# Kernel tuning notes

Hardware: AMD Instinct MI355X
Metric: run time of the kernel (lower is better)

Reference implementation:

```python
import jax, jax.numpy as jnp
import numpy as np

B, HIDDEN, NH, MAX_S = 8, 4096, 32, 4096
HD = HIDDEN // NH  # 128
POS = 2047  # current cache write position (tokens 0..POS-1 already cached)


def setup_inputs() -> dict:
    key = jax.random.key(0)
    ks = jax.random.split(key, 7)
    x = jax.random.normal(ks[0], (B, 1, HIDDEN), dtype=jnp.float32)
    cached_k = jax.random.normal(ks[1], (B, NH, MAX_S, HD), dtype=jnp.float32)
    cached_v = jax.random.normal(ks[2], (B, NH, MAX_S, HD), dtype=jnp.float32)
    scale = 0.02
    wq = jax.random.normal(ks[3], (HIDDEN, HIDDEN), dtype=jnp.float32) * scale
    wk = jax.random.normal(ks[4], (HIDDEN, HIDDEN), dtype=jnp.float32) * scale
    wv = jax.random.normal(ks[5], (HIDDEN, HIDDEN), dtype=jnp.float32) * scale
    wo = jax.random.normal(ks[6], (HIDDEN, HIDDEN), dtype=jnp.float32) * scale
    return {"x": x, "cached_k": cached_k, "cached_v": cached_v,
            "wq": wq, "wk": wk, "wv": wv, "wo": wo, "cached_pos": POS}


def reference(x, cached_k, cached_v, wq, wk, wv, wo, cached_pos):
    # Decode step: seq_len == 1 (is_training=False path of the torch module).
    b, s, hidden = x.shape  # s == 1
    # Projections (torch Linear: y = x @ W.T), reshape to [B, H, 1, D]
    q = (x @ wq.T).reshape(b, s, NH, HD).transpose(0, 2, 1, 3)
    k = (x @ wk.T).reshape(b, s, NH, HD).transpose(0, 2, 1, 3)
    v = (x @ wv.T).reshape(b, s, NH, HD).transpose(0, 2, 1, 3)
    # Append new token's K/V into the cache at cached_pos (static python int)
    ck = cached_k.at[:, :, cached_pos, :].set(k[:, :, 0, :])
    cv = cached_v.at[:, :, cached_pos, :].set(v[:, :, 0, :])
    # Attend over the valid prefix [0, cached_pos]
    kk = ck[:, :, :cached_pos + 1, :]  # [B, H, T, D]
    vv = cv[:, :, :cached_pos + 1, :]
    scores = jnp.einsum('bhqd,bhkd->bhqk', q, kk) / jnp.sqrt(jnp.float32(HD))
    att = jax.nn.softmax(scores, axis=-1)  # stable softmax == module's _softmax
    out = jnp.einsum('bhqk,bhkd->bhqd', att, vv)  # [B, H, 1, D]
    out = out.transpose(0, 2, 1, 3).reshape(b, s, hidden)
    return out @ wo.T
```

## Files before the change

### kernel.cpp

```cpp
#include <hip/hip_runtime.h>
#include <cmath>

#define B_     8
#define NH_    32
#define HD_    128
#define HID_   4096
#define MAXS_  4096
#define NPAIR_ (B_ * NH_)
#define NSPLIT_ 4
#define PSTR_  132
#define NEG_BIG_ (-1e30f)

typedef float f4_ __attribute__((ext_vector_type(4)));

__device__ __forceinline__ f4_ ntload4(const float* p) {
  return __builtin_nontemporal_load((const f4_*)p);
}
__device__ __forceinline__ f4_ ld4(const float* p) {
  return *(const f4_*)p;
}
__device__ __forceinline__ float dot4(f4_ a, f4_ b) {
  f4_ m = a * b;
  return m.x + m.y + m.z + m.w;
}

__global__ __launch_bounds__(64) void gemv8(
    const float* __restrict__ W0, const float* __restrict__ W1,
    const float* __restrict__ W2, const float* __restrict__ x,
    float* __restrict__ out, int nb_per_mat)
{
  const int bid = blockIdx.x;
  const int m   = bid / nb_per_mat;
  const int r0  = (bid % nb_per_mat) * 8;
  const float* __restrict__ W = (m == 0) ? W0 : ((m == 1) ? W1 : W2);
  float* o = out + m * (B_ * HID_);

  const int lane = threadIdx.x;

  float acc[8][8];
#pragma unroll
  for (int r = 0; r < 8; ++r)
#pragma unroll
    for (int b = 0; b < 8; ++b) acc[r][b] = 0.f;

  const float* Wp = W + (size_t)r0 * HID_ + lane * 4;
  const float* xp = x + lane * 4;

  f4_ wa[8], wb[8];
#pragma unroll
  for (int r = 0; r < 8; ++r) wa[r] = ld4(Wp + (size_t)r * HID_);

#pragma unroll 1
  for (int u = 0; u < 16; u += 2) {
    {
      const int j = u * 256;
      f4_ xv[8];
#pragma unroll
      for (int b = 0; b < 8; ++b) xv[b] = ld4(xp + b * HID_ + j);
#pragma unroll
      for (int r = 0; r < 8; ++r)
        wb[r] = ld4(Wp + (size_t)r * HID_ + j + 256);
#pragma unroll
      for (int r = 0; r < 8; ++r)
#pragma unroll
        for (int b = 0; b < 8; ++b) acc[r][b] += dot4(wa[r], xv[b]);
    }
    {
      const int j = (u + 1) * 256;
      f4_ xv[8];
#pragma unroll
      for (int b = 0; b < 8; ++b) xv[b] = ld4(xp + b * HID_ + j);
      if (u + 2 < 16) {
#pragma unroll
        for (int r = 0; r < 8; ++r)
          wa[r] = ld4(Wp + (size_t)r * HID_ + j + 256);
      }
#pragma unroll
      for (int r = 0; r < 8; ++r)
#pragma unroll
        for (int b = 0; b < 8; ++b) acc[r][b] += dot4(wb[r], xv[b]);
    }
  }

#pragma unroll
  for (int r = 0; r < 8; ++r)
#pragma unroll
    for (int b = 0; b < 8; ++b) {
      float v = acc[r][b];
#pragma unroll
      for (int off = 32; off; off >>= 1) v += __shfl_xor(v, off);
      acc[r][b] = v;
    }

  if (lane == 0) {
#pragma unroll
    for (int r = 0; r < 8; ++r)
#pragma unroll
      for (int b = 0; b < 8; ++b)
        o[(size_t)b * HID_ + r0 + r] = acc[r][b];
  }
}

__global__ __launch_bounds__(256, 4) void attn_partial(
    const float* __restrict__ qkv, const float* __restrict__ ck,
    const float* __restrict__ cv, const int* __restrict__ ppos,
    float* __restrict__ part)
{
  __shared__ float sm[4], sl[4];
  __shared__ float sacc[4][HD_];

  const int pos  = *ppos;
  const int bid  = blockIdx.x;
  const int pair = bid >> 2;
  const int s    = bid & (NSPLIT_ - 1);
  const int b    = pair >> 5;
  const int h    = pair & (NH_ - 1);
  const int w    = threadIdx.x >> 6;
  const int lane = threadIdx.x & 63;
  const int half = lane >> 5, l32 = lane & 31;
  const int k0   = s * 512 + w * 128;

  float m = NEG_BIG_, l = 0.f;
  f4_ acc = (f4_)0.f;

  if (k0 <= pos) {
    const float scale = 0.08838834764831845f;
    f4_ q4 = ld4(qkv + b * HID_ + h * HD_ + l32 * 4) * scale;
    const float* kfresh = qkv + B_ * HID_     + b * HID_ + h * HD_;
    const float* vfresh = qkv + 2 * B_ * HID_ + b * HID_ + h * HD_;
    const float* ckh = ck + ((size_t)(b * NH_ + h)) * MAXS_ * HD_;
    const float* cvh = cv + ((size_t)(b * NH_ + h)) * MAXS_ * HD_;

    for (int c = 0; c < 8; ++c) {
      const int kbase = k0 + c * 16;
      f4_ k4[8], v4[8];
#pragma unroll
      for (int j = 0; j < 8; ++j) {
        const int ki = kbase + 2 * j + half;
        const float* kp = (ki == pos) ? kfresh : (ckh + (size_t)ki * HD_);
        const float* vp = (ki == pos) ? vfresh : (cvh + (size_t)ki * HD_);
        k4[j] = ntload4(kp + l32 * 4);
        v4[j] = ntload4(vp + l32 * 4);
      }

      float sc[8];
#pragma unroll
      for (int j = 0; j < 8; ++j) sc[j] = dot4(q4, k4[j]);

#pragma unroll
      for (int off = 16; off >= 1; off >>= 1)
#pragma unroll
        for (int j = 0; j < 8; ++j) sc[j] += __shfl_xor(sc[j], off);

#pragma unroll
      for (int j = 0; j < 8; ++j) {
        const int ki = kbase + 2 * j + half;
        if (ki > pos) sc[j] = -INFINITY;
      }

      const float cm = fmaxf(fmaxf(fmaxf(sc[0], sc[1]), fmaxf(sc[2], sc[3])),
                             fmaxf(fmaxf(sc[4], sc[5]), fmaxf(sc[6], sc[7])));
      const float mn   = fmaxf(m, cm);
      const float corr = __expf(m - mn);
      float p[8], ps = 0.f;
#pragma unroll
      for (int j = 0; j < 8; ++j) { p[j] = __expf(sc[j] - mn); ps += p[j]; }
      l = l * corr + ps;
      acc *= corr;
#pragma unroll
      for (int j = 0; j < 8; ++j) acc += p[j] * v4[j];
      m = mn;
    }
  }

  const float mo = __shfl_xor(m, 32);
  const float lo = __shfl_xor(l, 32);
  f4_ ao;
  ao.x = __shfl_xor(acc.x, 32); ao.y = __shfl_xor(acc.y, 32);
  ao.z = __shfl_xor(acc.z, 32); ao.w = __shfl_xor(acc.w, 32);
  const float mm = fmaxf(m, mo);
  const float w0 = __expf(m - mm), w1 = __expf(mo - mm);
  const float lm = l * w0 + lo * w1;
  f4_ am = acc * w0 + ao * w1;

  if (half == 0) {
    *(f4_*)&sacc[w][l32 * 4] = am;
    if (l32 == 0) { sm[w] = mm; sl[w] = lm; }
  }
  __syncthreads();

  if (threadIdx.x < 32) {
    const int t = threadIdx.x;
    float mg = NEG_BIG_;
#pragma unroll
    for (int u = 0; u < 4; ++u)
      if (sl[u] > 0.f) mg = fmaxf(mg, sm[u]);
    float ls = 0.f;
    f4_ o = (f4_)0.f;
#pragma unroll
    for (int u = 0; u < 4; ++u)
      if (sl[u] > 0.f) {
        const float wu = __expf(sm[u] - mg);
        ls += sl[u] * wu;
        o  += wu * ld4(&sacc[u][t * 4]);
      }
    float* pb = part + (size_t)bid * PSTR_;
    *(f4_*)(pb + 4 + t * 4) = o;
    if (t == 0) { pb[0] = (ls > 0.f) ? mg : NEG_BIG_; pb[1] = ls; }
  }
}

__global__ __launch_bounds__(128) void attn_combine(
    const float* __restrict__ part, float* __restrict__ attnout)
{
  const int pair = blockIdx.x;
  const int d    = threadIdx.x;
  const float* pb = part + (size_t)pair * NSPLIT_ * PSTR_;

  float mg = NEG_BIG_;
#pragma unroll
  for (int u = 0; u < NSPLIT_; ++u) {
    const float lu = pb[u * PSTR_ + 1];
    if (lu > 0.f) mg = fmaxf(mg, pb[u * PSTR_]);
  }
  float ls = 0.f, o = 0.f;
#pragma unroll
  for (int u = 0; u < NSPLIT_; ++u) {
    const float lu = pb[u * PSTR_ + 1];
    if (lu > 0.f) {
      const float wu = __expf(pb[u * PSTR_] - mg);
      ls += lu * wu;
      o  += wu * pb[u * PSTR_ + 4 + d];
    }
  }
  attnout[pair * HD_ + d] = o / ls;
}

extern "C" void kernel_launch(void* const* d_in, const int* in_sizes, int n_in,
                              void* d_out, int out_size, void* d_ws, size_t ws_size,
                              hipStream_t stream) {
  const float* x  = (const float*)d_in[0];
  const float* ck = (const float*)d_in[1];
  const float* cv = (const float*)d_in[2];
  const float* wq = (const float*)d_in[3];
  const float* wk = (const float*)d_in[4];
  const float* wv = (const float*)d_in[5];
  const float* wo = (const float*)d_in[6];
  const int* pos  = (const int*)d_in[7];
  float* out = (float*)d_out;
  float* ws  = (float*)d_ws;

  float* qkv     = ws;
  float* part    = ws + 3 * B_ * HID_;
  float* attnout = part + NPAIR_ * NSPLIT_ * PSTR_;

  gemv8<<<3 * 512, 64, 0, stream>>>(wq, wk, wv, x, qkv, 512);
  attn_partial<<<NPAIR_ * NSPLIT_, 256, 0, stream>>>(qkv, ck, cv, pos, part);
  attn_combine<<<NPAIR_, 128, 0, stream>>>(part, attnout);
  gemv8<<<512, 64, 0, stream>>>(wo, wo, wo, attnout, out, 512);
}
```

Baseline: 178.5 us.

## Split-K the QKV and output GEMVs to raise block count

The QKV projection now splits the reduction dimension in two and the output projection in four, so more workgroups each stream a shorter slice of the weight rows. The QKV partial sums are added inside the attention kernel when loading q and the fresh k/v, and the output partials are reduced by a new small sum kernel. The fresh-token substitution in attention changes from pointer selection to loading from the cache and then overwriting the value. The split costs extra partial-result traffic and one more kernel launch.

```diff
diff --git a/kernel.cpp b/kernel.cpp
--- a/kernel.cpp
+++ b/kernel.cpp
@@ -9,6 +9,7 @@
 #define NPAIR_ (B_ * NH_)
 #define NSPLIT_ 4
 #define PSTR_  132
+#define QS_    (3 * B_ * HID_)
 #define NEG_BIG_ (-1e30f)
 
 typedef float f4_ __attribute__((ext_vector_type(4)));
@@ -24,18 +25,22 @@
   return m.x + m.y + m.z + m.w;
 }
 
-__global__ __launch_bounds__(64) void gemv8(
+template<int NSL>
+__global__ __launch_bounds__(64) void gemv_ks(
     const float* __restrict__ W0, const float* __restrict__ W1,
     const float* __restrict__ W2, const float* __restrict__ x,
-    float* __restrict__ out, int nb_per_mat)
-{
-  const int bid = blockIdx.x;
-  const int m   = bid / nb_per_mat;
-  const int r0  = (bid % nb_per_mat) * 8;
+    float* __restrict__ out, int nb_per_mat, int n_inner, int part_stride)
+{
+  const int bid   = blockIdx.x;
+  const int ks    = bid / n_inner;
+  const int inner = bid % n_inner;
+  const int m     = inner / nb_per_mat;
+  const int r0    = (inner % nb_per_mat) * 8;
   const float* __restrict__ W = (m == 0) ? W0 : ((m == 1) ? W1 : W2);
-  float* o = out + m * (B_ * HID_);
+  float* o = out + (size_t)ks * part_stride + m * (B_ * HID_);
 
   const int lane = threadIdx.x;
+  const int kofs = ks * NSL * 256;
 
   float acc[8][8];
 #pragma unroll
@@ -43,15 +48,15 @@
 #pragma unroll
     for (int b = 0; b < 8; ++b) acc[r][b] = 0.f;
 
-  const float* Wp = W + (size_t)r0 * HID_ + lane * 4;
-  const float* xp = x + lane * 4;
+  const float* Wp = W + (size_t)r0 * HID_ + kofs + lane * 4;
+  const float* xp = x + kofs + lane * 4;
 
   f4_ wa[8], wb[8];
 #pragma unroll
   for (int r = 0; r < 8; ++r) wa[r] = ld4(Wp + (size_t)r * HID_);
 
 #pragma unroll 1
-  for (int u = 0; u < 16; u += 2) {
+  for (int u = 0; u < NSL; u += 2) {
     {
       const int j = u * 256;
       f4_ xv[8];
@@ -70,7 +75,7 @@
       f4_ xv[8];
 #pragma unroll
       for (int b = 0; b < 8; ++b) xv[b] = ld4(xp + b * HID_ + j);
-      if (u + 2 < 16) {
+      if (u + 2 < NSL) {
 #pragma unroll
         for (int r = 0; r < 8; ++r)
           wa[r] = ld4(Wp + (size_t)r * HID_ + j + 256);
@@ -99,6 +104,16 @@
       for (int b = 0; b < 8; ++b)
         o[(size_t)b * HID_ + r0 + r] = acc[r][b];
   }
+}
+
+__global__ __launch_bounds__(256) void sum4(
+    const float* __restrict__ part, float* __restrict__ out)
+{
+  const int gid = blockIdx.x * 256 + threadIdx.x;
+  const int i = gid * 4;
+  f4_ v = ld4(part + i) + ld4(part + (B_ * HID_) + i)
+        + ld4(part + 2 * (B_ * HID_) + i) + ld4(part + 3 * (B_ * HID_) + i);
+  *(f4_*)(out + i) = v;
 }
 
 __global__ __launch_bounds__(256, 4) void attn_partial(
@@ -125,9 +140,10 @@
 
   if (k0 <= pos) {
     const float scale = 0.08838834764831845f;
-    f4_ q4 = ld4(qkv + b * HID_ + h * HD_ + l32 * 4) * scale;
-    const float* kfresh = qkv + B_ * HID_     + b * HID_ + h * HD_;
-    const float* vfresh = qkv + 2 * B_ * HID_ + b * HID_ + h * HD_;
+    const int hoff = b * HID_ + h * HD_ + l32 * 4;
+    f4_ q4  = (ld4(qkv + hoff) + ld4(qkv + QS_ + hoff)) * scale;
+    f4_ kf4 =  ld4(qkv + B_ * HID_ + hoff) + ld4(qkv + QS_ + B_ * HID_ + hoff);
+    f4_ vf4 =  ld4(qkv + 2 * B_ * HID_ + hoff) + ld4(qkv + QS_ + 2 * B_ * HID_ + hoff);
     const float* ckh = ck + ((size_t)(b * NH_ + h)) * MAXS_ * HD_;
     const float* cvh = cv + ((size_t)(b * NH_ + h)) * MAXS_ * HD_;
 
@@ -137,10 +153,13 @@
 #pragma unroll
       for (int j = 0; j < 8; ++j) {
         const int ki = kbase + 2 * j + half;
-        const float* kp = (ki == pos) ? kfresh : (ckh + (size_t)ki * HD_);
-        const float* vp = (ki == pos) ? vfresh : (cvh + (size_t)ki * HD_);
-        k4[j] = ntload4(kp + l32 * 4);
-        v4[j] = ntload4(vp + l32 * 4);
+        k4[j] = ntload4(ckh + (size_t)ki * HD_ + l32 * 4);
+        v4[j] = ntload4(cvh + (size_t)ki * HD_ + l32 * 4);
+      }
+#pragma unroll
+      for (int j = 0; j < 8; ++j) {
+        const int ki = kbase + 2 * j + half;
+        if (ki == pos) { k4[j] = kf4; v4[j] = vf4; }
       }
 
       float sc[8];
@@ -250,12 +269,16 @@
   float* out = (float*)d_out;
   float* ws  = (float*)d_ws;
 
-  float* qkv     = ws;
-  float* part    = ws + 3 * B_ * HID_;
+  float* qkvp    = ws;
+  float* part    = qkvp + 2 * QS_;
   float* attnout = part + NPAIR_ * NSPLIT_ * PSTR_;
-
-  gemv8<<<3 * 512, 64, 0, stream>>>(wq, wk, wv, x, qkv, 512);
-  attn_partial<<<NPAIR_ * NSPLIT_, 256, 0, stream>>>(qkv, ck, cv, pos, part);
+  float* wopart  = attnout + B_ * HID_;
+
+  gemv_ks<8><<<2 * 3 * 512, 64, 0, stream>>>(wq, wk, wv, x, qkvp,
+                                             512, 3 * 512, QS_);
+  attn_partial<<<NPAIR_ * NSPLIT_, 256, 0, stream>>>(qkvp, ck, cv, pos, part);
   attn_combine<<<NPAIR_, 128, 0, stream>>>(part, attnout);
-  gemv8<<<512, 64, 0, stream>>>(wo, wo, wo, attnout, out, 512);
-}
+  gemv_ks<4><<<4 * 512, 64, 0, stream>>>(wo, wo, wo, attnout, wopart,
+                                         512, 512, B_ * HID_);
+  sum4<<<(B_ * HID_) / (256 * 4), 256, 0, stream>>>(wopart, out);
+}
```

New measurement: 182.4 us. +2.2%, slower.
